# Kernel tuning notes

Measured on AMD Instinct MI355X. Metric: run time of the kernel, lower is better.

The kernel has to match this reference:

```python
import jax, jax.numpy as jnp
import numpy as np

N_NODES = 100000
IN_CH, HID_CH, OUT_CH = 128, 128, 64
N_EDGES = 1600000


def _gcn_conv(x, W, b, src, dst, num_nodes):
    """PyG GCNConv with gcn_norm(add_self_loops=True): adds one self-loop per
    node to the given edge set, symmetric deg^-1/2 normalization, then
    gather-scale-scatter of the linearly transformed features."""
    loop = jnp.arange(num_nodes)
    s = jnp.concatenate([src, loop])
    d = jnp.concatenate([dst, loop])
    # degree over targets (flow source_to_target), edge weights = 1
    deg = jax.ops.segment_sum(jnp.ones_like(s, x.dtype), d, num_segments=num_nodes)
    dinv = jnp.where(deg > 0, deg ** -0.5, 0.0)
    norm = dinv[s] * dinv[d]                      # [E']
    h = x @ W                                     # [N, out]
    msg = h[s] * norm[:, None]                    # [E', out] gather + scale
    out = jax.ops.segment_sum(msg, d, num_segments=num_nodes)  # scatter-add
    return out + b


def setup_inputs() -> dict:
    key = jax.random.key(0)
    k = jax.random.split(key, 6)
    x = jax.random.normal(k[0], (N_NODES, IN_CH), dtype=jnp.float32)
    edge_index = jax.random.randint(k[1], (2, N_EDGES), 0, N_NODES, dtype=jnp.int64)
    # Glorot-scale params
    W1 = jax.random.normal(k[2], (IN_CH, HID_CH), dtype=jnp.float32) * (2.0 / (IN_CH + HID_CH)) ** 0.5
    b1 = jnp.zeros((HID_CH,), dtype=jnp.float32)
    W2 = jax.random.normal(k[3], (HID_CH, OUT_CH), dtype=jnp.float32) * (2.0 / (HID_CH + OUT_CH)) ** 0.5
    b2 = jnp.zeros((OUT_CH,), dtype=jnp.float32)
    return {"x": x, "edge_index": edge_index, "W1": W1, "b1": b1, "W2": W2, "b2": b2}


def reference(x, edge_index, W1, b1, W2, b2):
    num_nodes = x.shape[0]
    loop = jnp.arange(num_nodes, dtype=edge_index.dtype)
    # wrapper-level add_self_loops (GCNConv adds another internally)
    src = jnp.concatenate([edge_index[0], loop])
    dst = jnp.concatenate([edge_index[1], loop])
    h = _gcn_conv(x, W1, b1, src, dst, num_nodes)
    h = jax.nn.relu(h)
    h = _gcn_conv(h, W2, b2, src, dst, num_nodes)
    return jax.nn.log_softmax(h, axis=1)
```

## Files before the change

### kernel.cpp

```cpp
#include <hip/hip_runtime.h>
#include <cstdint>
#include <cstddef>

#define IN_CH 128
#define HID_CH 128
#define OUT_CH 64
#define BSH 8
#define PB 4096

typedef unsigned int uint32;
typedef unsigned char uchar;
typedef short bf16x8 __attribute__((ext_vector_type(8)));
typedef float f32x4 __attribute__((ext_vector_type(4)));
typedef float f32x2 __attribute__((ext_vector_type(2)));

static __device__ __forceinline__ unsigned short f2bf(float f) {
    uint32 u = __float_as_uint(f);
    u += 0x7fffu + ((u >> 16) & 1u);
    return (unsigned short)(u >> 16);
}
static __device__ __forceinline__ uchar f2fp8(float f) {
    int p = __builtin_amdgcn_cvt_pk_fp8_f32(f, f, 0, false);
    return (uchar)(p & 0xff);
}

typedef const __attribute__((address_space(1))) char gch;
typedef __attribute__((address_space(3))) char lch;
static __device__ __forceinline__ void gload16(const void* g, void* l) {
    __builtin_amdgcn_global_load_lds((gch*)g, (lch*)l, 16, 0, 0);
}


__global__ __launch_bounds__(256) void bhist_wtrans(
    const int* __restrict__ dst, int* __restrict__ bcnt, int E, int NB, int gP,
    const float* __restrict__ W1, const float* __restrict__ W2,
    unsigned short* __restrict__ W1t, unsigned short* __restrict__ W2t) {
    if (blockIdx.x >= (uint32)gP) {
        int t = (blockIdx.x - gP) * 256 + threadIdx.x;
        if (t < 128 * 128) {
            int nc = t >> 7, k = t & 127;
            W1t[t] = f2bf(W1[k * 128 + nc]);
        }
        int u = t - 128 * 128;
        if (u >= 0 && u < 64 * 128) {
            int nc = u >> 7, k = u & 127;
            W2t[u] = f2bf(W2[k * 64 + nc]);
        }
        return;
    }
    __shared__ int h[512];
    int t = threadIdx.x;
    int e0 = blockIdx.x * PB;
    int cnt = min(PB, E - e0);
    for (int b = t; b < NB; b += 256) h[b] = 0;
    __syncthreads();
    for (int i = t; i < cnt; i += 256)
        atomicAdd(&h[dst[e0 + i] >> BSH], 1);
    __syncthreads();
    for (int b = t; b < NB; b += 256)
        if (h[b]) atomicAdd(&bcnt[b], h[b]);
}

__global__ void bscan(const int* __restrict__ bcnt, int* __restrict__ bbase,
                      int* __restrict__ bcur, int NB, int E) {
    __shared__ int s[512];
    int t = threadIdx.x;
    int v = (t < NB) ? bcnt[t] : 0;
    s[t] = v;
    __syncthreads();
    for (int o = 1; o < 512; o <<= 1) {
        int add = (t >= o) ? s[t - o] : 0;
        __syncthreads();
        s[t] += add;
        __syncthreads();
    }
    if (t < NB) { bbase[t] = s[t] - v; bcur[t] = 0; }
    if (t == 0) bbase[NB] = E;
}

__global__ __launch_bounds__(256) void part1(
    const int* __restrict__ src, const int* __restrict__ dst,
    const int* __restrict__ bbase, int* __restrict__ bcur,
    int2* __restrict__ pairBuf, int E, int NB) {
    __shared__ int2 pairs[PB];
    __shared__ int hist[512];
    __shared__ int base[512];
    int t = threadIdx.x;
    int e0 = blockIdx.x * PB;
    int cnt = min(PB, E - e0);
    for (int b = t; b < NB; b += 256) hist[b] = 0;
    __syncthreads();
    for (int i = t; i < cnt; i += 256) {
        int s = src[e0 + i], d = dst[e0 + i];
        pairs[i] = make_int2(s, d);
        atomicAdd(&hist[d >> BSH], 1);
    }
    __syncthreads();
    for (int b = t; b < NB; b += 256) {
        int h = hist[b];
        int gb = (h > 0) ? atomicAdd(&bcur[b], h) : 0;
        base[b] = bbase[b] + gb;
        hist[b] = 0;
    }
    __syncthreads();
    for (int i = t; i < cnt; i += 256) {
        int2 p = pairs[i];
        int b = p.y >> BSH;
        int q = base[b] + atomicAdd(&hist[b], 1);
        pairBuf[q] = p;
    }
}

__global__ __launch_bounds__(256) void bucket_build(
    const int2* __restrict__ pairBuf, const int* __restrict__ bbase,
    int* __restrict__ rowptr, int* __restrict__ deg, float* __restrict__ dinv,
    int* __restrict__ csr, int N) {
    __shared__ int cnt[256];
    __shared__ int loc[256];
    int b = blockIdx.x, t = threadIdx.x;
    int start = bbase[b], end = bbase[b + 1];
    cnt[t] = 0;
    __syncthreads();
    for (int i = start + t; i < end; i += 256)
        atomicAdd(&cnt[pairBuf[i].y & 255], 1);
    __syncthreads();
    int v = cnt[t];
    loc[t] = v;
    __syncthreads();
    for (int o = 1; o < 256; o <<= 1) {
        int add = (t >= o) ? loc[t - o] : 0;
        __syncthreads();
        loc[t] += add;
        __syncthreads();
    }
    int excl = loc[t] - v;
    int node = (b << BSH) + t;
    if (node < N) {
        rowptr[node] = start + excl;
        deg[node] = v;
        dinv[node] = rsqrtf((float)(v + 2));
    }
    __syncthreads();
    cnt[t] = excl;
    __syncthreads();
    for (int i = start + t; i < end; i += 256) {
        int2 p = pairBuf[i];
        int q = start + atomicAdd(&cnt[p.y & 255], 1);
        csr[q] = p.x;
    }
}


template <int OUT, bool AFP32>
__global__ __launch_bounds__(256) void gemm_mfma(
    const void* __restrict__ Av, const unsigned short* __restrict__ Wt,
    const float* __restrict__ dinv, uchar* __restrict__ C, int n, int nTiles) {
    constexpr int NT = OUT / 16;
    constexpr int ROWB = AFP32 ? 512 : 256;
    constexpr int TILEB = 64 * ROWB;
    constexpr int RNDS = TILEB / 4096;
    __shared__ unsigned short Ws[OUT * 136];
    __shared__ char As[TILEB];

    const int t = threadIdx.x;

    for (int i = t; i < OUT * 16; i += 256) {
        int rr = i >> 4, sq = i & 15;
        *(uint4*)&Ws[rr * 136 + sq * 8] = *(const uint4*)(Wt + rr * 128 + sq * 8);
    }

    const int w = t >> 6, l = t & 63;
    const int q = l >> 4, r16 = l & 15;
    const int rw = w * 16 + r16;
    const char* Ab = (const char*)Av;

    for (int tile = blockIdx.x; tile < nTiles; tile += gridDim.x) {
        const int row0 = tile * 64;

#pragma unroll
        for (int rnd = 0; rnd < RNDS; rnd++) {
            int p = rnd * 4096 + t * 16;
            int row = row0 + (AFP32 ? (p >> 9) : (p >> 8));
            int col = AFP32 ? (p & 511) : (p & 255);
            gload16(Ab + (size_t)min(row, n - 1) * ROWB + col, As + p);
        }
        __syncthreads();

        f32x4 acc[NT];
#pragma unroll
        for (int i = 0; i < NT; i++) acc[i] = (f32x4){0.f, 0.f, 0.f, 0.f};

#pragma unroll
        for (int s = 0; s < 4; s++) {
            const int k0 = s * 32 + q * 8;
            bf16x8 a;
            if (AFP32) {
                const float* Arow = (const float*)(As + rw * 512);
                float4 v0 = *(const float4*)(Arow + k0);
                float4 v1 = *(const float4*)(Arow + k0 + 4);
                a[0] = (short)f2bf(v0.x); a[1] = (short)f2bf(v0.y);
                a[2] = (short)f2bf(v0.z); a[3] = (short)f2bf(v0.w);
                a[4] = (short)f2bf(v1.x); a[5] = (short)f2bf(v1.y);
                a[6] = (short)f2bf(v1.z); a[7] = (short)f2bf(v1.w);
            } else {
                a = *(const bf16x8*)(As + rw * 256 + k0 * 2);
            }
#pragma unroll
            for (int nt = 0; nt < NT; nt++) {
                bf16x8 b = *(const bf16x8*)&Ws[(nt * 16 + r16) * 136 + k0];
                acc[nt] = __builtin_amdgcn_mfma_f32_16x16x32_bf16(a, b, acc[nt], 0, 0, 0);
            }
        }

        const int rbase = row0 + w * 16 + q * 4;
        float4 dv4 = *(const float4*)(dinv + rbase);
        float dva[4] = {dv4.x, dv4.y, dv4.z, dv4.w};
#pragma unroll
        for (int nt = 0; nt < NT; nt++) {
#pragma unroll
            for (int p = 0; p < 4; p++) {
                int rr = rbase + p;
                if (rr < n) C[(size_t)rr * OUT + nt * 16 + r16] = f2fp8(acc[nt][p] * dva[p]);
            }
        }
        __syncthreads();
    }
}


__global__ __launch_bounds__(256) void agg_relu_128(
    const uchar* __restrict__ H, const int* __restrict__ csr,
    const int* __restrict__ rowptr, const int* __restrict__ deg,
    const float* __restrict__ dinv, const float* __restrict__ bias,
    unsigned short* __restrict__ out, int n) {
    int v = blockIdx.x * 16 + (threadIdx.x >> 4);
    int hl = threadIdx.x & 15;
    int gsel = threadIdx.x & 48;
    bool valid = v < n;
    int vc = valid ? v : 0;
    int base = rowptr[vc];
    int cnt = valid ? deg[vc] : 0;
    const uint32 co = (uint32)(hl * 8);

    f32x2 A0 = (f32x2){0.f, 0.f}, A1 = A0, A2 = A0, A3 = A0;
    f32x2 B0 = A0, B1 = A0, B2 = A0, B3 = A0;

#define ACC128(h, s0, s1, s2, s3)                                   \
    {                                                               \
        s0 += __builtin_amdgcn_cvt_pk_f32_fp8((h).x, false);        \
        s1 += __builtin_amdgcn_cvt_pk_f32_fp8((h).x, true);         \
        s2 += __builtin_amdgcn_cvt_pk_f32_fp8((h).y, false);        \
        s3 += __builtin_amdgcn_cvt_pk_f32_fp8((h).y, true);         \
    }

    for (int j0 = 0; j0 < cnt; j0 += 16) {
        int nj = min(16, cnt - j0);
        int ul = 0;
        if (hl < nj) ul = csr[base + j0 + hl];
        int j = 0;
        for (; j + 8 <= nj; j += 8) {
            int u0 = __shfl(ul, (j + 0) | gsel), u1 = __shfl(ul, (j + 1) | gsel);
            int u2 = __shfl(ul, (j + 2) | gsel), u3 = __shfl(ul, (j + 3) | gsel);
            int u4 = __shfl(ul, (j + 4) | gsel), u5 = __shfl(ul, (j + 5) | gsel);
            int u6 = __shfl(ul, (j + 6) | gsel), u7 = __shfl(ul, (j + 7) | gsel);
            uint2 h0 = *(const uint2*)(H + (((uint32)u0 << 7) + co));
            uint2 h1 = *(const uint2*)(H + (((uint32)u1 << 7) + co));
            uint2 h2 = *(const uint2*)(H + (((uint32)u2 << 7) + co));
            uint2 h3 = *(const uint2*)(H + (((uint32)u3 << 7) + co));
            uint2 h4 = *(const uint2*)(H + (((uint32)u4 << 7) + co));
            uint2 h5 = *(const uint2*)(H + (((uint32)u5 << 7) + co));
            uint2 h6 = *(const uint2*)(H + (((uint32)u6 << 7) + co));
            uint2 h7 = *(const uint2*)(H + (((uint32)u7 << 7) + co));
            ACC128(h0, A0, A1, A2, A3);
            ACC128(h1, B0, B1, B2, B3);
            ACC128(h2, A0, A1, A2, A3);
            ACC128(h3, B0, B1, B2, B3);
            ACC128(h4, A0, A1, A2, A3);
            ACC128(h5, B0, B1, B2, B3);
            ACC128(h6, A0, A1, A2, A3);
            ACC128(h7, B0, B1, B2, B3);
        }
        for (; j + 4 <= nj; j += 4) {
            int u0 = __shfl(ul, (j + 0) | gsel), u1 = __shfl(ul, (j + 1) | gsel);
            int u2 = __shfl(ul, (j + 2) | gsel), u3 = __shfl(ul, (j + 3) | gsel);
            uint2 h0 = *(const uint2*)(H + (((uint32)u0 << 7) + co));
            uint2 h1 = *(const uint2*)(H + (((uint32)u1 << 7) + co));
            uint2 h2 = *(const uint2*)(H + (((uint32)u2 << 7) + co));
            uint2 h3 = *(const uint2*)(H + (((uint32)u3 << 7) + co));
            ACC128(h0, A0, A1, A2, A3);
            ACC128(h1, B0, B1, B2, B3);
            ACC128(h2, A0, A1, A2, A3);
            ACC128(h3, B0, B1, B2, B3);
        }
        for (; j < nj; j++) {
            int u = __shfl(ul, j | gsel);
            uint2 h = *(const uint2*)(H + (((uint32)u << 7) + co));
            ACC128(h, A0, A1, A2, A3);
        }
    }
#undef ACC128

    if (valid) {
        float dv = dinv[vc];
        uint2 hv = *(const uint2*)(H + (((uint32)vc << 7) + co));
        f32x2 s0 = __builtin_amdgcn_cvt_pk_f32_fp8(hv.x, false);
        f32x2 s1 = __builtin_amdgcn_cvt_pk_f32_fp8(hv.x, true);
        f32x2 s2 = __builtin_amdgcn_cvt_pk_f32_fp8(hv.y, false);
        f32x2 s3 = __builtin_amdgcn_cvt_pk_f32_fp8(hv.y, true);
        const f32x2* bp = (const f32x2*)(bias + hl * 8);
        f32x2 e0 = dv * ((A0 + B0) + 2.f * s0) + bp[0];
        f32x2 e1 = dv * ((A1 + B1) + 2.f * s1) + bp[1];
        f32x2 e2 = dv * ((A2 + B2) + 2.f * s2) + bp[2];
        f32x2 e3 = dv * ((A3 + B3) + 2.f * s3) + bp[3];
        float o0 = fmaxf(e0[0], 0.f), o1 = fmaxf(e0[1], 0.f);
        float o2 = fmaxf(e1[0], 0.f), o3 = fmaxf(e1[1], 0.f);
        float o4 = fmaxf(e2[0], 0.f), o5 = fmaxf(e2[1], 0.f);
        float o6 = fmaxf(e3[0], 0.f), o7 = fmaxf(e3[1], 0.f);
        uint4 pk;
        pk.x = (uint32)f2bf(o0) | ((uint32)f2bf(o1) << 16);
        pk.y = (uint32)f2bf(o2) | ((uint32)f2bf(o3) << 16);
        pk.z = (uint32)f2bf(o4) | ((uint32)f2bf(o5) << 16);
        pk.w = (uint32)f2bf(o6) | ((uint32)f2bf(o7) << 16);
        *(uint4*)(out + (size_t)vc * 128 + hl * 8) = pk;
    }
}

__global__ __launch_bounds__(256) void agg_lsm_64(
    const uchar* __restrict__ H, const int* __restrict__ csr,
    const int* __restrict__ rowptr, const int* __restrict__ deg,
    const float* __restrict__ dinv, const float* __restrict__ bias,
    float* __restrict__ out, int n) {
    int v = blockIdx.x * 16 + (threadIdx.x >> 4);
    int hl = threadIdx.x & 15;
    int gsel = threadIdx.x & 48;
    bool valid = v < n;
    int vc = valid ? v : 0;
    int base = rowptr[vc];
    int cnt = valid ? deg[vc] : 0;
    const uint32 co = (uint32)(hl * 4);

    f32x2 A0 = (f32x2){0.f, 0.f}, A1 = A0, B0 = A0, B1 = A0;

#define ACC64(h, s0, s1)                                            \
    {                                                               \
        s0 += __builtin_amdgcn_cvt_pk_f32_fp8((h), false);          \
        s1 += __builtin_amdgcn_cvt_pk_f32_fp8((h), true);           \
    }

    for (int j0 = 0; j0 < cnt; j0 += 16) {
        int nj = min(16, cnt - j0);
        int ul = 0;
        if (hl < nj) ul = csr[base + j0 + hl];
        int j = 0;
        for (; j + 8 <= nj; j += 8) {
            int u0 = __shfl(ul, (j + 0) | gsel), u1 = __shfl(ul, (j + 1) | gsel);
            int u2 = __shfl(ul, (j + 2) | gsel), u3 = __shfl(ul, (j + 3) | gsel);
            int u4 = __shfl(ul, (j + 4) | gsel), u5 = __shfl(ul, (j + 5) | gsel);
            int u6 = __shfl(ul, (j + 6) | gsel), u7 = __shfl(ul, (j + 7) | gsel);
            uint32 h0 = *(const uint32*)(H + (((uint32)u0 << 6) + co));
            uint32 h1 = *(const uint32*)(H + (((uint32)u1 << 6) + co));
            uint32 h2 = *(const uint32*)(H + (((uint32)u2 << 6) + co));
            uint32 h3 = *(const uint32*)(H + (((uint32)u3 << 6) + co));
            uint32 h4 = *(const uint32*)(H + (((uint32)u4 << 6) + co));
            uint32 h5 = *(const uint32*)(H + (((uint32)u5 << 6) + co));
            uint32 h6 = *(const uint32*)(H + (((uint32)u6 << 6) + co));
            uint32 h7 = *(const uint32*)(H + (((uint32)u7 << 6) + co));
            ACC64(h0, A0, A1);
            ACC64(h1, B0, B1);
            ACC64(h2, A0, A1);
            ACC64(h3, B0, B1);
            ACC64(h4, A0, A1);
            ACC64(h5, B0, B1);
            ACC64(h6, A0, A1);
            ACC64(h7, B0, B1);
        }
        for (; j + 4 <= nj; j += 4) {
            int u0 = __shfl(ul, (j + 0) | gsel), u1 = __shfl(ul, (j + 1) | gsel);
            int u2 = __shfl(ul, (j + 2) | gsel), u3 = __shfl(ul, (j + 3) | gsel);
            uint32 h0 = *(const uint32*)(H + (((uint32)u0 << 6) + co));
            uint32 h1 = *(const uint32*)(H + (((uint32)u1 << 6) + co));
            uint32 h2 = *(const uint32*)(H + (((uint32)u2 << 6) + co));
            uint32 h3 = *(const uint32*)(H + (((uint32)u3 << 6) + co));
            ACC64(h0, A0, A1);
            ACC64(h1, B0, B1);
            ACC64(h2, A0, A1);
            ACC64(h3, B0, B1);
        }
        for (; j < nj; j++) {
            int u = __shfl(ul, j | gsel);
            uint32 h = *(const uint32*)(H + (((uint32)u << 6) + co));
            ACC64(h, A0, A1);
        }
    }
#undef ACC64

    float dv = dinv[vc];
    uint32 hv = *(const uint32*)(H + (((uint32)vc << 6) + co));
    f32x2 s0 = __builtin_amdgcn_cvt_pk_f32_fp8(hv, false);
    f32x2 s1 = __builtin_amdgcn_cvt_pk_f32_fp8(hv, true);
    const f32x2* bp = (const f32x2*)(bias + hl * 4);
    f32x2 w0 = dv * ((A0 + B0) + 2.f * s0) + bp[0];
    f32x2 w1 = dv * ((A1 + B1) + 2.f * s1) + bp[1];
    float v0 = w0[0], v1 = w0[1], v2 = w1[0], v3 = w1[1];
    float m = fmaxf(fmaxf(v0, v1), fmaxf(v2, v3));
    for (int o = 8; o > 0; o >>= 1) m = fmaxf(m, __shfl_xor(m, o));
    float e = (__expf(v0 - m) + __expf(v1 - m)) + (__expf(v2 - m) + __expf(v3 - m));
    for (int o = 8; o > 0; o >>= 1) e += __shfl_xor(e, o);
    float ls = m + __logf(e);
    if (valid)
        *(float4*)(out + (size_t)vc * 64 + hl * 4) =
            make_float4(v0 - ls, v1 - ls, v2 - ls, v3 - ls);
}


extern "C" void kernel_launch(void* const* d_in, const int* in_sizes, int n_in,
                              void* d_out, int out_size, void* d_ws, size_t ws_size,
                              hipStream_t stream) {
    const float* x  = (const float*)d_in[0];
    const int*   ei = (const int*)d_in[1];
    const float* W1 = (const float*)d_in[2];
    const float* b1 = (const float*)d_in[3];
    const float* W2 = (const float*)d_in[4];
    const float* b2 = (const float*)d_in[5];
    float* out = (float*)d_out;

    const int N = in_sizes[0] / IN_CH;
    const int E = in_sizes[1] / 2;
    const int* src = ei;
    const int* dst = ei + E;
    const int NB = (N + 255) >> BSH;

    char* w = (char*)d_ws;
    size_t off = 0;
    auto alloc = [&](size_t bytes) -> char* {
        char* p = w + off;
        off = (off + bytes + 255) & ~(size_t)255;
        return p;
    };
    int*   deg    = (int*)alloc((size_t)N * 4);
    int*   rowptr = (int*)alloc((size_t)N * 4);
    int*   bcnt   = (int*)alloc(512 * 4);
    int*   bbase  = (int*)alloc(513 * 4);
    int*   bcur   = (int*)alloc(512 * 4);
    float* dinv   = (float*)alloc((size_t)N * 4 + 1024);
    int*   csr    = (int*)alloc((size_t)E * 4);
    unsigned short* W1t = (unsigned short*)alloc(128 * 128 * 2);
    unsigned short* W2t = (unsigned short*)alloc(64 * 128 * 2);
    uchar* H1  = (uchar*)alloc((size_t)N * HID_CH);
    unsigned short* A1b = (unsigned short*)alloc((size_t)N * HID_CH * 2);
    uchar* H2  = H1;
    int2*  pairBuf = (int2*)A1b;

    hipMemsetAsync(bcnt, 0, 512 * 4, stream);

    int gP = (E + PB - 1) / PB;

    bhist_wtrans<<<gP + 96, 256, 0, stream>>>(dst, bcnt, E, NB, gP, W1, W2, W1t, W2t);
    bscan<<<1, 512, 0, stream>>>(bcnt, bbase, bcur, NB, E);
    part1<<<gP, 256, 0, stream>>>(src, dst, bbase, bcur, pairBuf, E, NB);
    bucket_build<<<NB, 256, 0, stream>>>(pairBuf, bbase, rowptr, deg, dinv, csr, N);

    const int nTiles = (N + 63) / 64;
    const int gG = min(nTiles, 512);
    gemm_mfma<128, true><<<gG, 256, 0, stream>>>(x, W1t, dinv, H1, N, nTiles);
    agg_relu_128<<<(N + 15) / 16, 256, 0, stream>>>(H1, csr, rowptr, deg, dinv, b1, A1b, N);
    gemm_mfma<64, false><<<gG, 256, 0, stream>>>(A1b, W2t, dinv, H2, N, nTiles);
    agg_lsm_64<<<(N + 15) / 16, 256, 0, stream>>>(H2, csr, rowptr, deg, dinv, b2, out, N);
}
```

Measured before the change: 255.7 us.

## Fuse second-layer GEMM into first aggregation kernel and pack fp8 stores

Fuses the layer-2 linear transform into the layer-1 aggregation kernel. Each block stages its 16 aggregated bf16 rows in shared memory and runs MFMA against W2t to write fp8 H2 directly. This removes the bf16 intermediate round-trip through global memory and one kernel launch. The layer-1 GEMM swaps its MFMA operands so each lane holds one output row and writes packed 4-byte fp8 stores instead of single bytes. In exchange, W2t is read from global memory per block without LDS staging, and the aggregation kernel gains a barrier plus extra registers.

```diff
diff --git a/kernel.cpp b/kernel.cpp
--- a/kernel.cpp
+++ b/kernel.cpp
@@ -18,10 +18,6 @@
     uint32 u = __float_as_uint(f);
     u += 0x7fffu + ((u >> 16) & 1u);
     return (unsigned short)(u >> 16);
-}
-static __device__ __forceinline__ uchar f2fp8(float f) {
-    int p = __builtin_amdgcn_cvt_pk_fp8_f32(f, f, 0, false);
-    return (uchar)(p & 0xff);
 }
 
 typedef const __attribute__((address_space(1))) char gch;
@@ -151,20 +147,16 @@
 }
 
 
-template <int OUT, bool AFP32>
-__global__ __launch_bounds__(256) void gemm_mfma(
-    const void* __restrict__ Av, const unsigned short* __restrict__ Wt,
+__global__ __launch_bounds__(256) void gemm1_mfma(
+    const float* __restrict__ A, const unsigned short* __restrict__ Wt,
     const float* __restrict__ dinv, uchar* __restrict__ C, int n, int nTiles) {
-    constexpr int NT = OUT / 16;
-    constexpr int ROWB = AFP32 ? 512 : 256;
-    constexpr int TILEB = 64 * ROWB;
-    constexpr int RNDS = TILEB / 4096;
-    __shared__ unsigned short Ws[OUT * 136];
-    __shared__ char As[TILEB];
+    constexpr int NT = 8;
+    __shared__ unsigned short Ws[128 * 136];
+    __shared__ char As[64 * 512];
 
     const int t = threadIdx.x;
 
-    for (int i = t; i < OUT * 16; i += 256) {
+    for (int i = t; i < 128 * 16; i += 256) {
         int rr = i >> 4, sq = i & 15;
         *(uint4*)&Ws[rr * 136 + sq * 8] = *(const uint4*)(Wt + rr * 128 + sq * 8);
     }
@@ -172,17 +164,16 @@
     const int w = t >> 6, l = t & 63;
     const int q = l >> 4, r16 = l & 15;
     const int rw = w * 16 + r16;
-    const char* Ab = (const char*)Av;
 
     for (int tile = blockIdx.x; tile < nTiles; tile += gridDim.x) {
         const int row0 = tile * 64;
 
 #pragma unroll
-        for (int rnd = 0; rnd < RNDS; rnd++) {
+        for (int rnd = 0; rnd < 8; rnd++) {
             int p = rnd * 4096 + t * 16;
-            int row = row0 + (AFP32 ? (p >> 9) : (p >> 8));
-            int col = AFP32 ? (p & 511) : (p & 255);
-            gload16(Ab + (size_t)min(row, n - 1) * ROWB + col, As + p);
+            int row = row0 + (p >> 9);
+            int col = p & 511;
+            gload16((const char*)A + (size_t)min(row, n - 1) * 512 + col, As + p);
         }
         __syncthreads();
 
@@ -193,49 +184,48 @@
 #pragma unroll
         for (int s = 0; s < 4; s++) {
             const int k0 = s * 32 + q * 8;
-            bf16x8 a;
-            if (AFP32) {
-                const float* Arow = (const float*)(As + rw * 512);
-                float4 v0 = *(const float4*)(Arow + k0);
-                float4 v1 = *(const float4*)(Arow + k0 + 4);
-                a[0] = (short)f2bf(v0.x); a[1] = (short)f2bf(v0.y);
-                a[2] = (short)f2bf(v0.z); a[3] = (short)f2bf(v0.w);
-                a[4] = (short)f2bf(v1.x); a[5] = (short)f2bf(v1.y);
-                a[6] = (short)f2bf(v1.z); a[7] = (short)f2bf(v1.w);
-            } else {
-                a = *(const bf16x8*)(As + rw * 256 + k0 * 2);
+            const float* Arow = (const float*)(As + rw * 512);
+            float4 v0 = *(const float4*)(Arow + k0);
+            float4 v1 = *(const float4*)(Arow + k0 + 4);
+            bf16x8 xf;
+            xf[0] = (short)f2bf(v0.x); xf[1] = (short)f2bf(v0.y);
+            xf[2] = (short)f2bf(v0.z); xf[3] = (short)f2bf(v0.w);
+            xf[4] = (short)f2bf(v1.x); xf[5] = (short)f2bf(v1.y);
+            xf[6] = (short)f2bf(v1.z); xf[7] = (short)f2bf(v1.w);
+#pragma unroll
+            for (int nt = 0; nt < NT; nt++) {
+                bf16x8 wf = *(const bf16x8*)&Ws[(nt * 16 + r16) * 136 + k0];
+                acc[nt] = __builtin_amdgcn_mfma_f32_16x16x32_bf16(wf, xf, acc[nt], 0, 0, 0);
             }
-#pragma unroll
-            for (int nt = 0; nt < NT; nt++) {
-                bf16x8 b = *(const bf16x8*)&Ws[(nt * 16 + r16) * 136 + k0];
-                acc[nt] = __builtin_amdgcn_mfma_f32_16x16x32_bf16(a, b, acc[nt], 0, 0, 0);
-            }
-        }
-
-        const int rbase = row0 + w * 16 + q * 4;
-        float4 dv4 = *(const float4*)(dinv + rbase);
-        float dva[4] = {dv4.x, dv4.y, dv4.z, dv4.w};
+        }
+
+        const int node = row0 + rw;
+        const bool nv = node < n;
+        const float dv = dinv[min(node, n - 1)];
+        uchar* Crow = C + (size_t)node * 128;
 #pragma unroll
         for (int nt = 0; nt < NT; nt++) {
-#pragma unroll
-            for (int p = 0; p < 4; p++) {
-                int rr = rbase + p;
-                if (rr < n) C[(size_t)rr * OUT + nt * 16 + r16] = f2fp8(acc[nt][p] * dva[p]);
-            }
-        }
-        __syncthreads();
-    }
-}
-
-
-__global__ __launch_bounds__(256) void agg_relu_128(
+            int pk = 0;
+            pk = __builtin_amdgcn_cvt_pk_fp8_f32(acc[nt][0] * dv, acc[nt][1] * dv, pk, false);
+            pk = __builtin_amdgcn_cvt_pk_fp8_f32(acc[nt][2] * dv, acc[nt][3] * dv, pk, true);
+            if (nv) *(uint32*)(Crow + nt * 16 + q * 4) = (uint32)pk;
+        }
+        __syncthreads();
+    }
+}
+
+
+__global__ __launch_bounds__(256) void agg1_fused(
     const uchar* __restrict__ H, const int* __restrict__ csr,
     const int* __restrict__ rowptr, const int* __restrict__ deg,
     const float* __restrict__ dinv, const float* __restrict__ bias,
-    unsigned short* __restrict__ out, int n) {
-    int v = blockIdx.x * 16 + (threadIdx.x >> 4);
-    int hl = threadIdx.x & 15;
-    int gsel = threadIdx.x & 48;
+    const unsigned short* __restrict__ W2t, uchar* __restrict__ H2, int n) {
+    __shared__ unsigned short tile[16 * 136];
+    int t = threadIdx.x;
+    int g = t >> 4;
+    int v = blockIdx.x * 16 + g;
+    int hl = t & 15;
+    int gsel = t & 48;
     bool valid = v < n;
     int vc = valid ? v : 0;
     int base = rowptr[vc];
@@ -300,6 +290,7 @@
     }
 #undef ACC128
 
+    uint4 pk = make_uint4(0, 0, 0, 0);
     if (valid) {
         float dv = dinv[vc];
         uint2 hv = *(const uint2*)(H + (((uint32)vc << 7) + co));
@@ -316,12 +307,31 @@
         float o2 = fmaxf(e1[0], 0.f), o3 = fmaxf(e1[1], 0.f);
         float o4 = fmaxf(e2[0], 0.f), o5 = fmaxf(e2[1], 0.f);
         float o6 = fmaxf(e3[0], 0.f), o7 = fmaxf(e3[1], 0.f);
-        uint4 pk;
         pk.x = (uint32)f2bf(o0) | ((uint32)f2bf(o1) << 16);
         pk.y = (uint32)f2bf(o2) | ((uint32)f2bf(o3) << 16);
         pk.z = (uint32)f2bf(o4) | ((uint32)f2bf(o5) << 16);
         pk.w = (uint32)f2bf(o6) | ((uint32)f2bf(o7) << 16);
-        *(uint4*)(out + (size_t)vc * 128 + hl * 8) = pk;
+    }
+    *(uint4*)&tile[g * 136 + hl * 8] = pk;
+    __syncthreads();
+
+    const int w = t >> 6, l = t & 63;
+    const int q = l >> 4, r16 = l & 15;
+    f32x4 acc2 = (f32x4){0.f, 0.f, 0.f, 0.f};
+#pragma unroll
+    for (int s = 0; s < 4; s++) {
+        const int k0 = s * 32 + q * 8;
+        bf16x8 hf = *(const bf16x8*)&tile[r16 * 136 + k0];
+        bf16x8 wf = *(const bf16x8*)(W2t + (size_t)(w * 16 + r16) * 128 + k0);
+        acc2 = __builtin_amdgcn_mfma_f32_16x16x32_bf16(wf, hf, acc2, 0, 0, 0);
+    }
+    const int node = blockIdx.x * 16 + r16;
+    if (node < n) {
+        const float dv2 = dinv[node];
+        int pk2 = 0;
+        pk2 = __builtin_amdgcn_cvt_pk_fp8_f32(acc2[0] * dv2, acc2[1] * dv2, pk2, false);
+        pk2 = __builtin_amdgcn_cvt_pk_fp8_f32(acc2[2] * dv2, acc2[3] * dv2, pk2, true);
+        *(uint32*)(H2 + (size_t)node * 64 + w * 16 + q * 4) = (uint32)pk2;
     }
 }
 
@@ -447,9 +457,9 @@
     unsigned short* W1t = (unsigned short*)alloc(128 * 128 * 2);
     unsigned short* W2t = (unsigned short*)alloc(64 * 128 * 2);
     uchar* H1  = (uchar*)alloc((size_t)N * HID_CH);
-    unsigned short* A1b = (unsigned short*)alloc((size_t)N * HID_CH * 2);
-    uchar* H2  = H1;
-    int2*  pairBuf = (int2*)A1b;
+    char*  scratch = alloc((size_t)E * 8);
+    uchar* H2  = (uchar*)scratch;
+    int2*  pairBuf = (int2*)scratch;
 
     hipMemsetAsync(bcnt, 0, 512 * 4, stream);
 
@@ -462,8 +472,7 @@
 
     const int nTiles = (N + 63) / 64;
     const int gG = min(nTiles, 512);
-    gemm_mfma<128, true><<<gG, 256, 0, stream>>>(x, W1t, dinv, H1, N, nTiles);
-    agg_relu_128<<<(N + 15) / 16, 256, 0, stream>>>(H1, csr, rowptr, deg, dinv, b1, A1b, N);
-    gemm_mfma<64, false><<<gG, 256, 0, stream>>>(A1b, W2t, dinv, H2, N, nTiles);
+    gemm1_mfma<<<gG, 256, 0, stream>>>(x, W1t, dinv, H1, N, nTiles);
+    agg1_fused<<<(N + 15) / 16, 256, 0, stream>>>(H1, csr, rowptr, deg, dinv, b1, W2t, H2, N);
     agg_lsm_64<<<(N + 15) / 16, 256, 0, stream>>>(H2, csr, rowptr, deg, dinv, b2, out, N);
 }
```

Measured after the change: 242.4 us. 1.06x faster.
